# Optimization experiments

Hardware: AMD Instinct MI355X
Metric: run time of the kernel (lower is better)

## Reference

```python
import jax, jax.numpy as jnp
import numpy as np

N_HEADS = 16
WINDOW = 128
EPS = 1e-6
NEG_INF = -1e30  # effectively -inf after softmax in fp32


def setup_inputs() -> dict:
    key = jax.random.key(0)
    ks = jax.random.split(key, 5)
    B, T, D = 2, 2048, 1024
    scale = 1.0 / np.sqrt(D)
    return {
        "x": jax.random.normal(ks[0], (B, T, D), dtype=jnp.float32),
        "Wq": jax.random.normal(ks[1], (D, D), dtype=jnp.float32) * scale,
        "Wk": jax.random.normal(ks[2], (D, D), dtype=jnp.float32) * scale,
        "Wv": jax.random.normal(ks[3], (D, D), dtype=jnp.float32) * scale,
        "Wo": jax.random.normal(ks[4], (D, D), dtype=jnp.float32) * scale,
    }


def _l2norm(t):
    # torch F.normalize: t / max(||t||, eps)
    n = jnp.sqrt(jnp.sum(t * t, axis=-1, keepdims=True))
    return t / jnp.maximum(n, EPS)


def reference(x, Wq, Wk, Wv, Wo):
    B, T, D = x.shape
    H, hd = N_HEADS, D // N_HEADS
    # projections (torch Linear: x @ W.T), split heads -> [B, H, T, hd]
    def proj(W):
        return jnp.einsum('btd,ed->bte', x, W).reshape(B, T, H, hd).transpose(0, 2, 1, 3)
    q = _l2norm(proj(Wq))
    k = _l2norm(proj(Wk))
    v = proj(Wv)
    # scores [B, H, T, T] (no 1/sqrt(d) scale in the source)
    attn = jnp.einsum('bhqd,bhkd->bhqk', q, k)
    pos = jnp.arange(T)
    rel = pos[None, :] - pos[:, None]            # rel[i, j] = j - i
    mask = (rel < 0) | (rel >= WINDOW)           # allowed: 0 <= j-i < window
    base = jnp.linspace(0.0, 1.0, H, dtype=x.dtype)
    slopes = jnp.power(jnp.asarray(2.0, x.dtype), -(8.0 * base))  # [H]
    alibi = -jnp.abs(rel).astype(x.dtype)[None, :, :] * slopes[:, None, None]  # [H,T,T]
    bias = jnp.where(mask[None, :, :], jnp.asarray(NEG_INF, x.dtype), alibi)
    attn = jax.nn.softmax(attn + bias[None], axis=-1)
    out = jnp.einsum('bhqk,bhkd->bhqd', attn, v)
    out = out.transpose(0, 2, 1, 3).reshape(B, T, D)
    return jnp.einsum('btd,ed->bte', out, Wo)
```

## Files before the change

### kernel.cpp

```cpp
#include <hip/hip_runtime.h>
#include <hip/hip_bf16.h>

#define T_SEQ   2048
#define BATCH   2
#define DMODEL  1024
#define NHEADS  16
#define HDIM    64
#define WINDOW  128

typedef __attribute__((ext_vector_type(8))) short bf16x8;
typedef __attribute__((ext_vector_type(4))) float f32x4;

#define LGKM(n)  asm volatile("s_waitcnt lgkmcnt(" #n ")" ::: "memory")
#define VMCNT(n) asm volatile("s_waitcnt vmcnt(" #n ")" ::: "memory")
#define SCHEDB() __builtin_amdgcn_sched_barrier(0)
#define BAR()    __builtin_amdgcn_s_barrier()

__device__ inline void gld_lds16(const __hip_bfloat16* g, __hip_bfloat16* l) {
    __builtin_amdgcn_global_load_lds(
        (const __attribute__((address_space(1))) unsigned int*)g,
        (__attribute__((address_space(3))) unsigned int*)l, 16, 0, 0);
}

__device__ inline bf16x8 ds_readb128(const __hip_bfloat16* p) {
    bf16x8 r;
    asm volatile("ds_read_b128 %0, %1"
                 : "=v"(r)
                 : "v"((const __attribute__((address_space(3))) __hip_bfloat16*)p));
    return r;
}

__global__ __launch_bounds__(256) void cvt_kernel(
    const float* __restrict__ x,  const float* __restrict__ Wq,
    const float* __restrict__ Wk, const float* __restrict__ Wv,
    const float* __restrict__ Wo,
    __hip_bfloat16* __restrict__ xb, __hip_bfloat16* __restrict__ Wb)
{
    const int lid = blockIdx.x;
    const float* src;
    __hip_bfloat16* dst;
    int blk;
    if (lid < 2048) { src = x; dst = xb; blk = lid; }
    else {
        int slot = (lid - 2048) >> 9;
        blk = (lid - 2048) & 511;
        src = (slot == 0) ? Wq : (slot == 1) ? Wk : (slot == 2) ? Wv : Wo;
        dst = Wb + (size_t)slot * 1024 * 1024;
    }
    int i = (blk * 256 + threadIdx.x) * 8;
    float4 a = *(const float4*)(src + i);
    float4 b = *(const float4*)(src + i + 4);
    __hip_bfloat16 pk[8] = {
        __float2bfloat16(a.x), __float2bfloat16(a.y),
        __float2bfloat16(a.z), __float2bfloat16(a.w),
        __float2bfloat16(b.x), __float2bfloat16(b.y),
        __float2bfloat16(b.z), __float2bfloat16(b.w)};
    *(uint4*)(dst + i) = *(uint4*)pk;
}

__global__ __launch_bounds__(256, 2) void gemm_qkv(
    const __hip_bfloat16* __restrict__ A,
    const __hip_bfloat16* __restrict__ Wp,
    __hip_bfloat16* __restrict__ C0,
    __hip_bfloat16* __restrict__ C1,
    __hip_bfloat16* __restrict__ C2)
{
    const int lid   = blockIdx.x;
    const int wgid  = (lid & 7) * 96 + (lid >> 3);
    const int bn    = wgid % 24;
    const int bm    = wgid / 24;
    const int m0    = bm * 128;
    const int n0    = bn * 128;
    const int z     = n0 >> 10;
    const int cbase = n0 & 1023;

    __shared__ __hip_bfloat16 S[2][2][128 * 64];

    const int t    = threadIdx.x;
    const int lane = t & 63;
    const int wv   = t >> 6;
    const int lrow = lane & 15;
    const int quad = lane >> 4;
    const int wm   = (wv >> 1) * 64;
    const int wn   = (wv & 1) * 64;
    const int drow = lane >> 3;
    const int sl   = lane & 7;

    f32x4 acc[4][4];
#pragma unroll
    for (int i = 0; i < 4; ++i)
#pragma unroll
        for (int j = 0; j < 4; ++j)
            acc[i][j] = (f32x4){0.f, 0.f, 0.f, 0.f};

    auto STAGE = [&](int tile, int buf) {
        const int k0 = tile << 6;
#pragma unroll
        for (int inst = 0; inst < 4; ++inst) {
            int r0 = wv * 32 + inst * 8;
            int r  = r0 + drow;
            int gcx = (sl - r) & 7;
            gld_lds16(A + (size_t)(m0 + r) * DMODEL + k0 + gcx * 8,
                      &S[buf][0][r0 * 64]);
        }
#pragma unroll
        for (int inst = 0; inst < 4; ++inst) {
            int r0 = wv * 32 + inst * 8;
            int r  = r0 + drow;
            int gcx = (sl - r) & 7;
            gld_lds16(Wp + (size_t)(n0 + r) * DMODEL + k0 + gcx * 8,
                      &S[buf][1][r0 * 64]);
        }
    };

    auto RDA = [&](int buf, int mi, int kc) -> bf16x8 {
        int r = wm + mi * 16 + lrow;
        return ds_readb128(&S[buf][0][r * 64 + (((kc + r) & 7) << 3)]);
    };
    auto RDB = [&](int buf, int ni, int kc) -> bf16x8 {
        int r = wn + ni * 16 + lrow;
        return ds_readb128(&S[buf][1][r * 64 + (((kc + r) & 7) << 3)]);
    };

    bf16x8 a0[4], b0[4], a1[4], b1[4];

    STAGE(0, 0);
    VMCNT(0);
    BAR();
#pragma unroll
    for (int mi = 0; mi < 4; ++mi) a0[mi] = RDA(0, mi, quad);
#pragma unroll
    for (int ni = 0; ni < 4; ++ni) b0[ni] = RDB(0, ni, quad);

#pragma unroll 2
    for (int tt = 0; tt < 16; ++tt) {
        const int cur = tt & 1, nxt = cur ^ 1;
        if (tt < 15) STAGE(tt + 1, nxt);
#pragma unroll
        for (int mi = 0; mi < 4; ++mi) a1[mi] = RDA(cur, mi, 4 + quad);
#pragma unroll
        for (int ni = 0; ni < 4; ++ni) b1[ni] = RDB(cur, ni, 4 + quad);
        LGKM(8); SCHEDB();
        __builtin_amdgcn_s_setprio(1);
#pragma unroll
        for (int mi = 0; mi < 4; ++mi)
#pragma unroll
            for (int ni = 0; ni < 4; ++ni)
                acc[mi][ni] = __builtin_amdgcn_mfma_f32_16x16x32_bf16(
                    a0[mi], b0[ni], acc[mi][ni], 0, 0, 0);
        __builtin_amdgcn_s_setprio(0);
        VMCNT(0);
        LGKM(0); SCHEDB();
        BAR();
        if (tt < 15) {
#pragma unroll
            for (int mi = 0; mi < 4; ++mi) a0[mi] = RDA(nxt, mi, quad);
#pragma unroll
            for (int ni = 0; ni < 4; ++ni) b0[ni] = RDB(nxt, ni, quad);
        }
        __builtin_amdgcn_s_setprio(1);
#pragma unroll
        for (int mi = 0; mi < 4; ++mi)
#pragma unroll
            for (int ni = 0; ni < 4; ++ni)
                acc[mi][ni] = __builtin_amdgcn_mfma_f32_16x16x32_bf16(
                    a1[mi], b1[ni], acc[mi][ni], 0, 0, 0);
        __builtin_amdgcn_s_setprio(0);
    }

    if (z != 2) {
#pragma unroll
        for (int mi = 0; mi < 4; ++mi) {
#pragma unroll
            for (int rr = 0; rr < 4; ++rr) {
                float ss = 0.f;
#pragma unroll
                for (int ni = 0; ni < 4; ++ni)
                    ss += acc[mi][ni][rr] * acc[mi][ni][rr];
                ss += __shfl_xor(ss, 1);
                ss += __shfl_xor(ss, 2);
                ss += __shfl_xor(ss, 4);
                ss += __shfl_xor(ss, 8);
                float inv = 1.0f / fmaxf(sqrtf(ss), 1e-6f);
#pragma unroll
                for (int ni = 0; ni < 4; ++ni)
                    acc[mi][ni][rr] *= inv;
            }
        }
    }

    __hip_bfloat16* C = (z == 0) ? C0 : (z == 1) ? C1 : C2;
#pragma unroll
    for (int mi = 0; mi < 4; ++mi) {
#pragma unroll
        for (int rr = 0; rr < 4; ++rr) {
            int row = m0 + wm + mi * 16 + quad * 4 + rr;
            __hip_bfloat16* Crow = C + (size_t)row * DMODEL + cbase + wn + lrow;
#pragma unroll
            for (int ni = 0; ni < 4; ++ni)
                Crow[ni * 16] = __float2bfloat16(acc[mi][ni][rr]);
        }
    }
}

__global__ __launch_bounds__(256, 2) void gemm_o(
    const __hip_bfloat16* __restrict__ A,
    const __hip_bfloat16* __restrict__ W,
    float* __restrict__ C)
{
    const int lid  = blockIdx.x;
    const int wgid = (lid & 7) * 64 + (lid >> 3);
    const int bn   = wgid & 7;
    const int bm   = wgid >> 3;
    const int m0   = bm * 64;
    const int n0   = bn * 128;

    __shared__ __hip_bfloat16 SA[2][64 * 64];
    __shared__ __hip_bfloat16 SB[2][128 * 64];

    const int t    = threadIdx.x;
    const int lane = t & 63;
    const int wv   = t >> 6;
    const int lrow = lane & 15;
    const int quad = lane >> 4;
    const int wm   = (wv >> 1) * 32;
    const int wn   = (wv & 1) * 64;
    const int drow = lane >> 3;
    const int sl   = lane & 7;

    f32x4 acc[2][4];
#pragma unroll
    for (int i = 0; i < 2; ++i)
#pragma unroll
        for (int j = 0; j < 4; ++j)
            acc[i][j] = (f32x4){0.f, 0.f, 0.f, 0.f};

    auto STAGE = [&](int tile, int buf) {
        const int k0 = tile << 6;
#pragma unroll
        for (int inst = 0; inst < 2; ++inst) {
            int r0 = wv * 16 + inst * 8;
            int r  = r0 + drow;
            int gcx = (sl - r) & 7;
            gld_lds16(A + (size_t)(m0 + r) * DMODEL + k0 + gcx * 8,
                      &SA[buf][r0 * 64]);
        }
#pragma unroll
        for (int inst = 0; inst < 4; ++inst) {
            int r0 = wv * 32 + inst * 8;
            int r  = r0 + drow;
            int gcx = (sl - r) & 7;
            gld_lds16(W + (size_t)(n0 + r) * DMODEL + k0 + gcx * 8,
                      &SB[buf][r0 * 64]);
        }
    };

    auto RDA = [&](int buf, int mi, int kc) -> bf16x8 {
        int r = wm + mi * 16 + lrow;
        return ds_readb128(&SA[buf][r * 64 + (((kc + r) & 7) << 3)]);
    };
    auto RDB = [&](int buf, int ni, int kc) -> bf16x8 {
        int r = wn + ni * 16 + lrow;
        return ds_readb128(&SB[buf][r * 64 + (((kc + r) & 7) << 3)]);
    };

    bf16x8 a0[2], b0[4], a1[2], b1[4];

    STAGE(0, 0);
    VMCNT(0);
    BAR();
#pragma unroll
    for (int mi = 0; mi < 2; ++mi) a0[mi] = RDA(0, mi, quad);
#pragma unroll
    for (int ni = 0; ni < 4; ++ni) b0[ni] = RDB(0, ni, quad);

#pragma unroll 2
    for (int tt = 0; tt < 16; ++tt) {
        const int cur = tt & 1, nxt = cur ^ 1;
        if (tt < 15) STAGE(tt + 1, nxt);
#pragma unroll
        for (int mi = 0; mi < 2; ++mi) a1[mi] = RDA(cur, mi, 4 + quad);
#pragma unroll
        for (int ni = 0; ni < 4; ++ni) b1[ni] = RDB(cur, ni, 4 + quad);
        LGKM(6); SCHEDB();
        __builtin_amdgcn_s_setprio(1);
#pragma unroll
        for (int mi = 0; mi < 2; ++mi)
#pragma unroll
            for (int ni = 0; ni < 4; ++ni)
                acc[mi][ni] = __builtin_amdgcn_mfma_f32_16x16x32_bf16(
                    a0[mi], b0[ni], acc[mi][ni], 0, 0, 0);
        __builtin_amdgcn_s_setprio(0);
        VMCNT(0);
        LGKM(0); SCHEDB();
        BAR();
        if (tt < 15) {
#pragma unroll
            for (int mi = 0; mi < 2; ++mi) a0[mi] = RDA(nxt, mi, quad);
#pragma unroll
            for (int ni = 0; ni < 4; ++ni) b0[ni] = RDB(nxt, ni, quad);
        }
        __builtin_amdgcn_s_setprio(1);
#pragma unroll
        for (int mi = 0; mi < 2; ++mi)
#pragma unroll
            for (int ni = 0; ni < 4; ++ni)
                acc[mi][ni] = __builtin_amdgcn_mfma_f32_16x16x32_bf16(
                    a1[mi], b1[ni], acc[mi][ni], 0, 0, 0);
        __builtin_amdgcn_s_setprio(0);
    }

#pragma unroll
    for (int mi = 0; mi < 2; ++mi) {
#pragma unroll
        for (int rr = 0; rr < 4; ++rr) {
            int row = m0 + wm + mi * 16 + quad * 4 + rr;
            float* Crow = C + (size_t)row * DMODEL + n0 + wn + lrow;
#pragma unroll
            for (int ni = 0; ni < 4; ++ni)
                Crow[ni * 16] = acc[mi][ni][rr];
        }
    }
}

__global__ __launch_bounds__(512) void attn_kernel(
    const __hip_bfloat16* __restrict__ Q,
    const __hip_bfloat16* __restrict__ K,
    const __hip_bfloat16* __restrict__ V,
    __hip_bfloat16* __restrict__ O)
{
    const int qb = blockIdx.x * 128;
    const int h  = blockIdx.y;
    const int b  = blockIdx.z;

    __shared__ __hip_bfloat16 KsP[8 * 16 * 168];
    __shared__ __hip_bfloat16 Vt[64 * 264];

    const size_t base = ((size_t)b * T_SEQ) * DMODEL + h * HDIM;
    const int t    = threadIdx.x;
    const int lane = t & 63;
    const int w    = t >> 6;
    const int col  = lane & 15;
    const int quad = lane >> 4;

    {
        const int drow = lane >> 3, sl = lane & 7;
#pragma unroll
        for (int inst = 0; inst < 4; inst++) {
            int r0 = w * 32 + inst * 8;
            int r  = r0 + drow;
            int gcx = (sl - r) & 7;
            int j  = min(qb + r, T_SEQ - 1);
            gld_lds16(K + base + (size_t)j * DMODEL + gcx * 8, &KsP[r0 * 64]);
        }
    }

    const __hip_bfloat16* qp = Q + base + (size_t)(qb + w * 16 + col) * DMODEL + quad * 8;
    bf16x8 qf0 = *(const bf16x8*)(qp);
    bf16x8 qf1 = *(const bf16x8*)(qp + 32);

    {
        int c  = t & 7;
        int b0 = (t >> 3) & 31;
        int hf = t >> 8;
        int sg = (b0 & ~7) | ((b0 + c) & 7);
        unsigned short m[8][4];
#pragma unroll
        for (int i = 0; i < 4; i++) {
            int j = min(qb + b0 * 8 + hf * 4 + i, T_SEQ - 1);
            uint4 u = *(const uint4*)(V + base + (size_t)j * DMODEL + c * 8);
            unsigned short tmp[8];
            *(uint4*)tmp = u;
#pragma unroll
            for (int e = 0; e < 8; e++) m[e][i] = tmp[e];
        }
#pragma unroll
        for (int e = 0; e < 8; e++)
            *(uint2*)&Vt[(c * 8 + e) * 264 + sg * 8 + hf * 4] = *(uint2*)m[e];
    }
    if (t < 64) {
        uint4 zz = {0, 0, 0, 0};
        *(uint4*)&Vt[t * 264 + 256] = zz;
    }
    __syncthreads();

    const float slope = exp2f(-8.0f * (float)h / 15.0f);

    f32x4 sc[9];
#pragma unroll
    for (int kt = 0; kt < 9; kt++) {
        sc[kt] = (f32x4){0.f, 0.f, 0.f, 0.f};
        int r = w * 16 + kt * 16 + col;
        bf16x8 kb0 = *(const bf16x8*)&KsP[r * 64 + ((quad     + r) & 7) * 8];
        bf16x8 kb1 = *(const bf16x8*)&KsP[r * 64 + ((quad + 4 + r) & 7) * 8];
        sc[kt] = __builtin_amdgcn_mfma_f32_16x16x32_bf16(qf0, kb0, sc[kt], 0, 0, 0);
        sc[kt] = __builtin_amdgcn_mfma_f32_16x16x32_bf16(qf1, kb1, sc[kt], 0, 0, 0);
    }

    float mx[4] = {-3e38f, -3e38f, -3e38f, -3e38f};
#pragma unroll
    for (int kt = 0; kt < 9; kt++) {
#pragma unroll
        for (int r = 0; r < 4; r++) {
            int ql  = quad * 4 + r;
            int rel = kt * 16 + col - ql;
            int ka  = qb + w * 16 + kt * 16 + col;
            bool valid = (rel >= 0) && (rel < WINDOW) && (ka < T_SEQ);
            float v = valid ? (sc[kt][r] - (float)rel * slope) : -1e30f;
            sc[kt][r] = v;
            mx[r] = fmaxf(mx[r], v);
        }
    }
#pragma unroll
    for (int r = 0; r < 4; r++) {
        mx[r] = fmaxf(mx[r], __shfl_xor(mx[r], 1));
        mx[r] = fmaxf(mx[r], __shfl_xor(mx[r], 2));
        mx[r] = fmaxf(mx[r], __shfl_xor(mx[r], 4));
        mx[r] = fmaxf(mx[r], __shfl_xor(mx[r], 8));
    }
    float sm[4] = {0.f, 0.f, 0.f, 0.f};
#pragma unroll
    for (int kt = 0; kt < 9; kt++) {
#pragma unroll
        for (int r = 0; r < 4; r++) {
            float e = __expf(sc[kt][r] - mx[r]);
            sc[kt][r] = e;
            sm[r] += e;
        }
    }
#pragma unroll
    for (int r = 0; r < 4; r++) {
        sm[r] += __shfl_xor(sm[r], 1);
        sm[r] += __shfl_xor(sm[r], 2);
        sm[r] += __shfl_xor(sm[r], 4);
        sm[r] += __shfl_xor(sm[r], 8);
        sm[r] = 1.0f / sm[r];
    }

    __syncthreads();
    __hip_bfloat16* Ps = KsP + w * (16 * 168);
#pragma unroll
    for (int kt = 0; kt < 9; kt++)
#pragma unroll
        for (int r = 0; r < 4; r++)
            Ps[(quad * 4 + r) * 168 + kt * 16 + col] = __float2bfloat16(sc[kt][r] * sm[r]);
#pragma unroll
    for (int i = 0; i < 4; i++)
        Ps[(lane & 15) * 168 + 144 + quad * 4 + i] = __float2bfloat16(0.f);
    __syncthreads();

    f32x4 o[4];
#pragma unroll
    for (int nd = 0; nd < 4; nd++) o[nd] = (f32x4){0.f, 0.f, 0.f, 0.f};
#pragma unroll
    for (int kc = 0; kc < 5; kc++) {
        bf16x8 pf = *(const bf16x8*)&Ps[col * 168 + kc * 32 + quad * 8];
        int bblk = w * 2 + kc * 4 + quad;
#pragma unroll
        for (int nd = 0; nd < 4; nd++) {
            int d  = nd * 16 + col;
            int sg = (bblk < 32) ? ((bblk & ~7) | ((bblk + (d >> 3)) & 7)) : 32;
            bf16x8 vf = *(const bf16x8*)&Vt[d * 264 + sg * 8];
            o[nd] = __builtin_amdgcn_mfma_f32_16x16x32_bf16(pf, vf, o[nd], 0, 0, 0);
        }
    }

#pragma unroll
    for (int r = 0; r < 4; r++) {
        __hip_bfloat16* op = O + base + (size_t)(qb + w * 16 + quad * 4 + r) * DMODEL + col;
#pragma unroll
        for (int nd = 0; nd < 4; nd++)
            op[nd * 16] = __float2bfloat16(o[nd][r]);
    }
}

extern "C" void kernel_launch(void* const* d_in, const int* in_sizes, int n_in,
                              void* d_out, int out_size, void* d_ws, size_t ws_size,
                              hipStream_t stream)
{
    const float* x  = (const float*)d_in[0];
    const float* Wq = (const float*)d_in[1];
    const float* Wk = (const float*)d_in[2];
    const float* Wv = (const float*)d_in[3];
    const float* Wo = (const float*)d_in[4];
    float* out = (float*)d_out;

    const size_t MT = (size_t)BATCH * T_SEQ;
    __hip_bfloat16* Qw = (__hip_bfloat16*)d_ws;
    __hip_bfloat16* Kw = Qw + MT * DMODEL;
    __hip_bfloat16* Vw = Kw + MT * DMODEL;
    __hip_bfloat16* XA = Vw + MT * DMODEL;
    __hip_bfloat16* Wb = XA + MT * DMODEL;

    cvt_kernel<<<4096, 256, 0, stream>>>(x, Wq, Wk, Wv, Wo, XA, Wb);

    gemm_qkv<<<dim3(768), 256, 0, stream>>>(XA, Wb, Qw, Kw, Vw);

    dim3 g2(T_SEQ / 128, NHEADS, BATCH);
    attn_kernel<<<g2, 512, 0, stream>>>(Qw, Kw, Vw, XA);

    gemm_o<<<dim3(512), 256, 0, stream>>>(XA, Wb + 3 * 1024 * 1024, out);
}
```

Before: 148.8 us.

## Pre-swizzle operands into MFMA fragment layout and load GEMM fragments directly from global

The convert kernel now writes x and the weights in a fragment-tiled layout matching the 16x16x32 MFMA operand order, and attention writes its output in the same layout. Both GEMMs drop the LDS staging, barriers and waitcnt asm and instead issue direct 128-bit global loads into registers with simple register double-buffering. The QKV GEMM also gets a new XCD-aware tile mapping and launch bounds raised to 3 waves per SIMD. One __syncthreads in attention is removed. This trades LDS traffic and synchronization for more global/L2 traffic, since tiles are no longer shared across waves through LDS. Dropping the barrier also risks a race on the P tile.

```diff
diff --git a/kernel.cpp b/kernel.cpp
--- a/kernel.cpp
+++ b/kernel.cpp
@@ -11,24 +11,12 @@
 typedef __attribute__((ext_vector_type(8))) short bf16x8;
 typedef __attribute__((ext_vector_type(4))) float f32x4;
 
-#define LGKM(n)  asm volatile("s_waitcnt lgkmcnt(" #n ")" ::: "memory")
-#define VMCNT(n) asm volatile("s_waitcnt vmcnt(" #n ")" ::: "memory")
-#define SCHEDB() __builtin_amdgcn_sched_barrier(0)
-#define BAR()    __builtin_amdgcn_s_barrier()
-
 __device__ inline void gld_lds16(const __hip_bfloat16* g, __hip_bfloat16* l) {
     __builtin_amdgcn_global_load_lds(
         (const __attribute__((address_space(1))) unsigned int*)g,
         (__attribute__((address_space(3))) unsigned int*)l, 16, 0, 0);
 }
 
-__device__ inline bf16x8 ds_readb128(const __hip_bfloat16* p) {
-    bf16x8 r;
-    asm volatile("ds_read_b128 %0, %1"
-                 : "=v"(r)
-                 : "v"((const __attribute__((address_space(3))) __hip_bfloat16*)p));
-    return r;
-}
 
 __global__ __launch_bounds__(256) void cvt_kernel(
     const float* __restrict__ x,  const float* __restrict__ Wq,
@@ -39,42 +27,48 @@
     const int lid = blockIdx.x;
     const float* src;
     __hip_bfloat16* dst;
-    int blk;
-    if (lid < 2048) { src = x; dst = xb; blk = lid; }
+    int ublk;
+    if (lid < 2048) { src = x; dst = xb; ublk = lid; }
     else {
         int slot = (lid - 2048) >> 9;
-        blk = (lid - 2048) & 511;
+        ublk = (lid - 2048) & 511;
         src = (slot == 0) ? Wq : (slot == 1) ? Wk : (slot == 2) ? Wv : Wo;
         dst = Wb + (size_t)slot * 1024 * 1024;
     }
-    int i = (blk * 256 + threadIdx.x) * 8;
-    float4 a = *(const float4*)(src + i);
-    float4 b = *(const float4*)(src + i + 4);
+    const int u    = ublk * 256 + threadIdx.x;
+    const int lrow = u & 15;
+    const int quad = (u >> 4) & 3;
+    const int g    = u >> 6;
+    const int k32  = g & 31;
+    const int t16  = g >> 5;
+    const int row  = t16 * 16 + lrow;
+    const int k    = k32 * 32 + quad * 8;
+
+    const float* sp = src + (size_t)row * 1024 + k;
+    float4 a = *(const float4*)sp;
+    float4 b = *(const float4*)(sp + 4);
     __hip_bfloat16 pk[8] = {
         __float2bfloat16(a.x), __float2bfloat16(a.y),
         __float2bfloat16(a.z), __float2bfloat16(a.w),
         __float2bfloat16(b.x), __float2bfloat16(b.y),
         __float2bfloat16(b.z), __float2bfloat16(b.w)};
-    *(uint4*)(dst + i) = *(uint4*)pk;
-}
-
-__global__ __launch_bounds__(256, 2) void gemm_qkv(
-    const __hip_bfloat16* __restrict__ A,
-    const __hip_bfloat16* __restrict__ Wp,
+    *(uint4*)(dst + (size_t)u * 8) = *(uint4*)pk;
+}
+
+__global__ __launch_bounds__(256, 3) void gemm_qkv(
+    const __hip_bfloat16* __restrict__ Af,
+    const __hip_bfloat16* __restrict__ Bf,
     __hip_bfloat16* __restrict__ C0,
     __hip_bfloat16* __restrict__ C1,
     __hip_bfloat16* __restrict__ C2)
 {
-    const int lid   = blockIdx.x;
-    const int wgid  = (lid & 7) * 96 + (lid >> 3);
-    const int bn    = wgid % 24;
-    const int bm    = wgid / 24;
-    const int m0    = bm * 128;
-    const int n0    = bn * 128;
-    const int z     = n0 >> 10;
-    const int cbase = n0 & 1023;
-
-    __shared__ __hip_bfloat16 S[2][2][128 * 64];
+    const int lid = blockIdx.x;
+    const int xcd = lid & 7;
+    const int s   = lid >> 3;
+    const int bm  = (xcd & 3) * 8 + s / 12;
+    const int bn  = (xcd >> 2) * 12 + s % 12;
+    const int m0 = bm * 128, n0 = bn * 128;
+    const int z = n0 >> 10, cbase = n0 & 1023;
 
     const int t    = threadIdx.x;
     const int lane = t & 63;
@@ -83,8 +77,9 @@
     const int quad = lane >> 4;
     const int wm   = (wv >> 1) * 64;
     const int wn   = (wv & 1) * 64;
-    const int drow = lane >> 3;
-    const int sl   = lane & 7;
+
+    const __hip_bfloat16* Ab = Af + (((size_t)((m0 + wm) >> 4) * 32) * 64 + lane) * 8;
+    const __hip_bfloat16* Bb = Bf + (((size_t)((n0 + wn) >> 4) * 32) * 64 + lane) * 8;
 
     f32x4 acc[4][4];
 #pragma unroll
@@ -93,79 +88,37 @@
         for (int j = 0; j < 4; ++j)
             acc[i][j] = (f32x4){0.f, 0.f, 0.f, 0.f};
 
-    auto STAGE = [&](int tile, int buf) {
-        const int k0 = tile << 6;
-#pragma unroll
-        for (int inst = 0; inst < 4; ++inst) {
-            int r0 = wv * 32 + inst * 8;
-            int r  = r0 + drow;
-            int gcx = (sl - r) & 7;
-            gld_lds16(A + (size_t)(m0 + r) * DMODEL + k0 + gcx * 8,
-                      &S[buf][0][r0 * 64]);
-        }
-#pragma unroll
-        for (int inst = 0; inst < 4; ++inst) {
-            int r0 = wv * 32 + inst * 8;
-            int r  = r0 + drow;
-            int gcx = (sl - r) & 7;
-            gld_lds16(Wp + (size_t)(n0 + r) * DMODEL + k0 + gcx * 8,
-                      &S[buf][1][r0 * 64]);
-        }
+    bf16x8 a0[4], b0[4], a1[4], b1[4];
+
+    auto LDA = [&](bf16x8* d, int ss) {
+#pragma unroll
+        for (int i = 0; i < 4; ++i)
+            d[i] = *(const bf16x8*)(Ab + ((size_t)(i * 32 + ss)) * 512);
     };
-
-    auto RDA = [&](int buf, int mi, int kc) -> bf16x8 {
-        int r = wm + mi * 16 + lrow;
-        return ds_readb128(&S[buf][0][r * 64 + (((kc + r) & 7) << 3)]);
+    auto LDB = [&](bf16x8* d, int ss) {
+#pragma unroll
+        for (int i = 0; i < 4; ++i)
+            d[i] = *(const bf16x8*)(Bb + ((size_t)(i * 32 + ss)) * 512);
     };
-    auto RDB = [&](int buf, int ni, int kc) -> bf16x8 {
-        int r = wn + ni * 16 + lrow;
-        return ds_readb128(&S[buf][1][r * 64 + (((kc + r) & 7) << 3)]);
-    };
-
-    bf16x8 a0[4], b0[4], a1[4], b1[4];
-
-    STAGE(0, 0);
-    VMCNT(0);
-    BAR();
-#pragma unroll
-    for (int mi = 0; mi < 4; ++mi) a0[mi] = RDA(0, mi, quad);
-#pragma unroll
-    for (int ni = 0; ni < 4; ++ni) b0[ni] = RDB(0, ni, quad);
-
-#pragma unroll 2
-    for (int tt = 0; tt < 16; ++tt) {
-        const int cur = tt & 1, nxt = cur ^ 1;
-        if (tt < 15) STAGE(tt + 1, nxt);
-#pragma unroll
-        for (int mi = 0; mi < 4; ++mi) a1[mi] = RDA(cur, mi, 4 + quad);
-#pragma unroll
-        for (int ni = 0; ni < 4; ++ni) b1[ni] = RDB(cur, ni, 4 + quad);
-        LGKM(8); SCHEDB();
-        __builtin_amdgcn_s_setprio(1);
+
+    LDA(a0, 0); LDB(b0, 0);
+
+    for (int ss = 0; ss < 32; ss += 2) {
+        LDA(a1, ss + 1); LDB(b1, ss + 1);
 #pragma unroll
         for (int mi = 0; mi < 4; ++mi)
 #pragma unroll
             for (int ni = 0; ni < 4; ++ni)
                 acc[mi][ni] = __builtin_amdgcn_mfma_f32_16x16x32_bf16(
                     a0[mi], b0[ni], acc[mi][ni], 0, 0, 0);
-        __builtin_amdgcn_s_setprio(0);
-        VMCNT(0);
-        LGKM(0); SCHEDB();
-        BAR();
-        if (tt < 15) {
-#pragma unroll
-            for (int mi = 0; mi < 4; ++mi) a0[mi] = RDA(nxt, mi, quad);
-#pragma unroll
-            for (int ni = 0; ni < 4; ++ni) b0[ni] = RDB(nxt, ni, quad);
-        }
-        __builtin_amdgcn_s_setprio(1);
+        const int s2 = (ss + 2 < 32) ? ss + 2 : 31;
+        LDA(a0, s2); LDB(b0, s2);
 #pragma unroll
         for (int mi = 0; mi < 4; ++mi)
 #pragma unroll
             for (int ni = 0; ni < 4; ++ni)
                 acc[mi][ni] = __builtin_amdgcn_mfma_f32_16x16x32_bf16(
                     a1[mi], b1[ni], acc[mi][ni], 0, 0, 0);
-        __builtin_amdgcn_s_setprio(0);
     }
 
     if (z != 2) {
@@ -173,15 +126,15 @@
         for (int mi = 0; mi < 4; ++mi) {
 #pragma unroll
             for (int rr = 0; rr < 4; ++rr) {
-                float ss = 0.f;
+                float ss2 = 0.f;
 #pragma unroll
                 for (int ni = 0; ni < 4; ++ni)
-                    ss += acc[mi][ni][rr] * acc[mi][ni][rr];
-                ss += __shfl_xor(ss, 1);
-                ss += __shfl_xor(ss, 2);
-                ss += __shfl_xor(ss, 4);
-                ss += __shfl_xor(ss, 8);
-                float inv = 1.0f / fmaxf(sqrtf(ss), 1e-6f);
+                    ss2 += acc[mi][ni][rr] * acc[mi][ni][rr];
+                ss2 += __shfl_xor(ss2, 1);
+                ss2 += __shfl_xor(ss2, 2);
+                ss2 += __shfl_xor(ss2, 4);
+                ss2 += __shfl_xor(ss2, 8);
+                float inv = 1.0f / fmaxf(sqrtf(ss2), 1e-6f);
 #pragma unroll
                 for (int ni = 0; ni < 4; ++ni)
                     acc[mi][ni][rr] *= inv;
@@ -204,19 +157,16 @@
 }
 
 __global__ __launch_bounds__(256, 2) void gemm_o(
-    const __hip_bfloat16* __restrict__ A,
-    const __hip_bfloat16* __restrict__ W,
+    const __hip_bfloat16* __restrict__ Af,
+    const __hip_bfloat16* __restrict__ Bf,
     float* __restrict__ C)
 {
     const int lid  = blockIdx.x;
     const int wgid = (lid & 7) * 64 + (lid >> 3);
+    const int bm   = wgid >> 3;
     const int bn   = wgid & 7;
-    const int bm   = wgid >> 3;
     const int m0   = bm * 64;
     const int n0   = bn * 128;
-
-    __shared__ __hip_bfloat16 SA[2][64 * 64];
-    __shared__ __hip_bfloat16 SB[2][128 * 64];
 
     const int t    = threadIdx.x;
     const int lane = t & 63;
@@ -225,8 +175,9 @@
     const int quad = lane >> 4;
     const int wm   = (wv >> 1) * 32;
     const int wn   = (wv & 1) * 64;
-    const int drow = lane >> 3;
-    const int sl   = lane & 7;
+
+    const __hip_bfloat16* Ab = Af + (((size_t)((m0 + wm) >> 4) * 32) * 64 + lane) * 8;
+    const __hip_bfloat16* Bb = Bf + (((size_t)((n0 + wn) >> 4) * 32) * 64 + lane) * 8;
 
     f32x4 acc[2][4];
 #pragma unroll
@@ -235,79 +186,37 @@
         for (int j = 0; j < 4; ++j)
             acc[i][j] = (f32x4){0.f, 0.f, 0.f, 0.f};
 
-    auto STAGE = [&](int tile, int buf) {
-        const int k0 = tile << 6;
-#pragma unroll
-        for (int inst = 0; inst < 2; ++inst) {
-            int r0 = wv * 16 + inst * 8;
-            int r  = r0 + drow;
-            int gcx = (sl - r) & 7;
-            gld_lds16(A + (size_t)(m0 + r) * DMODEL + k0 + gcx * 8,
-                      &SA[buf][r0 * 64]);
-        }
-#pragma unroll
-        for (int inst = 0; inst < 4; ++inst) {
-            int r0 = wv * 32 + inst * 8;
-            int r  = r0 + drow;
-            int gcx = (sl - r) & 7;
-            gld_lds16(W + (size_t)(n0 + r) * DMODEL + k0 + gcx * 8,
-                      &SB[buf][r0 * 64]);
-        }
+    bf16x8 a0[2], b0[4], a1[2], b1[4];
+
+    auto LDA = [&](bf16x8* d, int ss) {
+#pragma unroll
+        for (int i = 0; i < 2; ++i)
+            d[i] = *(const bf16x8*)(Ab + ((size_t)(i * 32 + ss)) * 512);
     };
-
-    auto RDA = [&](int buf, int mi, int kc) -> bf16x8 {
-        int r = wm + mi * 16 + lrow;
-        return ds_readb128(&SA[buf][r * 64 + (((kc + r) & 7) << 3)]);
+    auto LDB = [&](bf16x8* d, int ss) {
+#pragma unroll
+        for (int i = 0; i < 4; ++i)
+            d[i] = *(const bf16x8*)(Bb + ((size_t)(i * 32 + ss)) * 512);
     };
-    auto RDB = [&](int buf, int ni, int kc) -> bf16x8 {
-        int r = wn + ni * 16 + lrow;
-        return ds_readb128(&SB[buf][r * 64 + (((kc + r) & 7) << 3)]);
-    };
-
-    bf16x8 a0[2], b0[4], a1[2], b1[4];
-
-    STAGE(0, 0);
-    VMCNT(0);
-    BAR();
-#pragma unroll
-    for (int mi = 0; mi < 2; ++mi) a0[mi] = RDA(0, mi, quad);
-#pragma unroll
-    for (int ni = 0; ni < 4; ++ni) b0[ni] = RDB(0, ni, quad);
-
-#pragma unroll 2
-    for (int tt = 0; tt < 16; ++tt) {
-        const int cur = tt & 1, nxt = cur ^ 1;
-        if (tt < 15) STAGE(tt + 1, nxt);
-#pragma unroll
-        for (int mi = 0; mi < 2; ++mi) a1[mi] = RDA(cur, mi, 4 + quad);
-#pragma unroll
-        for (int ni = 0; ni < 4; ++ni) b1[ni] = RDB(cur, ni, 4 + quad);
-        LGKM(6); SCHEDB();
-        __builtin_amdgcn_s_setprio(1);
+
+    LDA(a0, 0); LDB(b0, 0);
+
+    for (int ss = 0; ss < 32; ss += 2) {
+        LDA(a1, ss + 1); LDB(b1, ss + 1);
 #pragma unroll
         for (int mi = 0; mi < 2; ++mi)
 #pragma unroll
             for (int ni = 0; ni < 4; ++ni)
                 acc[mi][ni] = __builtin_amdgcn_mfma_f32_16x16x32_bf16(
                     a0[mi], b0[ni], acc[mi][ni], 0, 0, 0);
-        __builtin_amdgcn_s_setprio(0);
-        VMCNT(0);
-        LGKM(0); SCHEDB();
-        BAR();
-        if (tt < 15) {
-#pragma unroll
-            for (int mi = 0; mi < 2; ++mi) a0[mi] = RDA(nxt, mi, quad);
-#pragma unroll
-            for (int ni = 0; ni < 4; ++ni) b0[ni] = RDB(nxt, ni, quad);
-        }
-        __builtin_amdgcn_s_setprio(1);
+        const int s2 = (ss + 2 < 32) ? ss + 2 : 31;
+        LDA(a0, s2); LDB(b0, s2);
 #pragma unroll
         for (int mi = 0; mi < 2; ++mi)
 #pragma unroll
             for (int ni = 0; ni < 4; ++ni)
                 acc[mi][ni] = __builtin_amdgcn_mfma_f32_16x16x32_bf16(
                     a1[mi], b1[ni], acc[mi][ni], 0, 0, 0);
-        __builtin_amdgcn_s_setprio(0);
     }
 
 #pragma unroll
@@ -447,7 +356,6 @@
 #pragma unroll
     for (int i = 0; i < 4; i++)
         Ps[(lane & 15) * 168 + 144 + quad * 4 + i] = __float2bfloat16(0.f);
-    __syncthreads();
 
     f32x4 o[4];
 #pragma unroll
@@ -467,10 +375,15 @@
 
 #pragma unroll
     for (int r = 0; r < 4; r++) {
-        __hip_bfloat16* op = O + base + (size_t)(qb + w * 16 + quad * 4 + r) * DMODEL + col;
-#pragma unroll
-        for (int nd = 0; nd < 4; nd++)
-            op[nd * 16] = __float2bfloat16(o[nd][r]);
+        int row_g = b * T_SEQ + qb + w * 16 + quad * 4 + r;
+        int rt = row_g >> 4, rl = row_g & 15;
+#pragma unroll
+        for (int nd = 0; nd < 4; nd++) {
+            int k_g = h * HDIM + nd * 16 + col;
+            size_t idx = (((size_t)rt * 32 + (k_g >> 5)) * 64
+                          + ((k_g >> 3) & 3) * 16 + rl) * 8 + (k_g & 7);
+            O[idx] = __float2bfloat16(o[nd][r]);
+        }
     }
 }
 
```

Measured after the change: 152.4 us. 2.4% more time.
